# Performance work log

Hardware: AMD Instinct MI355X
Metric: run time of the kernel (lower is better)

The kernel has to match this reference:

```python
import jax, jax.numpy as jnp
import numpy as np

B, S, D = 2, 2048, 1024
E, K, F = 8, 2, 4 * 1024  # num_experts, top_k, fc_rate*embed_dim
T = B * S


def setup_inputs() -> dict:
    key = jax.random.key(0)
    ks = jax.random.split(key, 8)
    w = lambda k, shape: jax.random.normal(k, shape, jnp.float32) * 0.02
    return {
        "hidden_states": jax.random.normal(ks[0], (B, S, D), jnp.float32),
        "noise": jax.random.normal(ks[1], (T, E), jnp.float32),  # randn_like in router
        "Wg": w(ks[2], (D, E)), "bg": jnp.zeros((E,), jnp.float32),
        "Wn": w(ks[3], (D, E)), "bn": jnp.zeros((E,), jnp.float32),
        "W1": w(ks[4], (E, D, F)), "b1": jnp.zeros((E, F), jnp.float32),
        "W2": w(ks[5], (E, F, D)), "b2": jnp.zeros((E, D), jnp.float32),
    }


def reference(hidden_states, noise, Wg, bg, Wn, bn, W1, b1, W2, b2):
    b, s, d = hidden_states.shape
    x = hidden_states.reshape(-1, d)  # [T, D]

    # --- NoisyTopkRouter ---
    gate_logits = x @ Wg + bg                        # [T, E]
    noise_logits = x @ Wn + bn                       # [T, E]
    noisy_logits = gate_logits + noise * jax.nn.softplus(noise_logits)
    rw = jax.nn.softmax(noisy_logits.astype(jnp.float32), axis=-1)
    top_w, top_i = jax.lax.top_k(rw, K)              # [T, K]
    top_w = top_w / top_w.sum(-1, keepdims=True)
    top_w = top_w.astype(x.dtype)

    # Dense per-token combine coefficients: coef[t,e] = sum_k top_w[t,k]*[top_i[t,k]==e]
    tok = jnp.arange(x.shape[0])[:, None]
    coef = jnp.zeros((x.shape[0], E), x.dtype).at[tok, top_i].add(top_w)  # [T, E]

    # --- Experts: Linear -> GELU(exact) -> Linear (dropout = identity, eval mode) ---
    h = jax.nn.gelu(jnp.einsum('td,edf->tef', x, W1) + b1, approximate=False)  # [T,E,F]
    y = jnp.einsum('tef,efd->ted', h, W2) + b2                                  # [T,E,D]
    out = jnp.einsum('ted,te->td', y, coef)                                     # [T,D]

    return out.reshape(b, s, d), noisy_logits, gate_logits
```

## Files before the change

kernel.cpp:

```cpp
#include <hip/hip_runtime.h>
#include <hip/hip_bf16.h>

#define T_TOK 4096
#define D_DIM 1024
#define E_NUM 8
#define F_DIM 4096
#define NPAIR 8192

#define BM 128
#define BN 128
#define BK 64

typedef float f32x4 __attribute__((ext_vector_type(4)));
typedef __bf16 bf16x8 __attribute__((ext_vector_type(8)));
typedef unsigned short u16x8 __attribute__((ext_vector_type(8)));

__device__ __forceinline__ unsigned short f2bf(float f) {
    unsigned int u = __float_as_uint(f);
    u += 0x7fffu + ((u >> 16) & 1u);
    return (unsigned short)(u >> 16);
}

typedef const __attribute__((address_space(1))) void GV;
typedef __attribute__((address_space(3))) void LV;

__device__ __forceinline__ void load_lds16(const void* g, void* l) {
    __builtin_amdgcn_global_load_lds((GV*)g, (LV*)l, 16, 0, 0);
}

__device__ __forceinline__ bf16x8 lds_frag(const unsigned short* S, int row, int cs) {
    int byte = row * (BK * 2) + ((cs * 2) ^ ((row & 7) << 4));
    return *(const bf16x8*)((const char*)S + byte);
}

__global__ __launch_bounds__(256) void router_kernel(
    const float* __restrict__ x, const float* __restrict__ noise,
    const float* __restrict__ Wg, const float* __restrict__ bg,
    const float* __restrict__ Wn, const float* __restrict__ bn,
    float* __restrict__ out_noisy, float* __restrict__ out_gate,
    int* __restrict__ tk_idx, float* __restrict__ tk_w)
{
    int lane = threadIdx.x & 63;
    int t = blockIdx.x * 4 + (threadIdx.x >> 6);
    const float* xr = x + (size_t)t * D_DIM;

    float ag[E_NUM] = {}, an[E_NUM] = {};
    for (int it = 0; it < D_DIM / 64; ++it) {
        int d = it * 64 + lane;
        float xv = xr[d];
        float4 g0 = *(const float4*)(Wg + (size_t)d * E_NUM);
        float4 g1 = *(const float4*)(Wg + (size_t)d * E_NUM + 4);
        float4 m0 = *(const float4*)(Wn + (size_t)d * E_NUM);
        float4 m1 = *(const float4*)(Wn + (size_t)d * E_NUM + 4);
        ag[0] += xv * g0.x; ag[1] += xv * g0.y; ag[2] += xv * g0.z; ag[3] += xv * g0.w;
        ag[4] += xv * g1.x; ag[5] += xv * g1.y; ag[6] += xv * g1.z; ag[7] += xv * g1.w;
        an[0] += xv * m0.x; an[1] += xv * m0.y; an[2] += xv * m0.z; an[3] += xv * m0.w;
        an[4] += xv * m1.x; an[5] += xv * m1.y; an[6] += xv * m1.z; an[7] += xv * m1.w;
    }
    #pragma unroll
    for (int off = 32; off > 0; off >>= 1) {
        #pragma unroll
        for (int e = 0; e < E_NUM; ++e) {
            ag[e] += __shfl_xor(ag[e], off);
            an[e] += __shfl_xor(an[e], off);
        }
    }
    if (lane == 0) {
        float nz[E_NUM];
        #pragma unroll
        for (int e = 0; e < E_NUM; ++e) {
            float g = ag[e] + bg[e];
            float nn = an[e] + bn[e];
            float sp = fmaxf(nn, 0.f) + log1pf(expf(-fabsf(nn)));
            float z = g + noise[(size_t)t * E_NUM + e] * sp;
            out_gate[(size_t)t * E_NUM + e] = g;
            out_noisy[(size_t)t * E_NUM + e] = z;
            nz[e] = z;
        }
        int e0 = 0;
        #pragma unroll
        for (int e = 1; e < E_NUM; ++e) if (nz[e] > nz[e0]) e0 = e;
        int e1 = (e0 == 0) ? 1 : 0;
        #pragma unroll
        for (int e = 0; e < E_NUM; ++e) if (e != e0 && nz[e] > nz[e1]) e1 = e;
        float b = expf(nz[e1] - nz[e0]);
        float w0 = 1.f / (1.f + b);
        float w1 = b / (1.f + b);
        tk_idx[t * 2] = e0;  tk_idx[t * 2 + 1] = e1;
        tk_w[t * 2] = w0;    tk_w[t * 2 + 1] = w1;
    }
}

__global__ __launch_bounds__(256) void scan_scatter_kernel(
    const int* __restrict__ tk_idx,
    int* __restrict__ perm, int* __restrict__ meta)
{
    __shared__ int cnt[256][E_NUM];
    __shared__ int soff[E_NUM];
    int tid = threadIdx.x;
    const int PPT = NPAIR / 256;
    int p0 = tid * PPT;

    int c[E_NUM] = {};
    for (int i = 0; i < PPT; ++i) c[tk_idx[p0 + i]]++;
    #pragma unroll
    for (int e = 0; e < E_NUM; ++e) cnt[tid][e] = c[e];
    __syncthreads();

    if (tid < E_NUM) {
        int s = 0;
        for (int j = 0; j < 256; ++j) { int v = cnt[j][tid]; cnt[j][tid] = s; s += v; }
        soff[tid] = s;
    }
    __syncthreads();

    if (tid == 0) {
        int off = 0, nt = 0;
        for (int e = 0; e < E_NUM; ++e) {
            int ce = soff[e];
            meta[1 + e] = off;
            meta[9 + e] = ce;
            for (int j = 0; j < ce; j += BM) {
                meta[32 + nt]  = e;
                meta[160 + nt] = off + j;
                meta[288 + nt] = off + ce;
                nt++;
            }
            off += ce;
        }
        meta[0] = nt;
    }
    __syncthreads();
    if (tid < E_NUM) soff[tid] = meta[1 + tid];
    __syncthreads();

    int pos[E_NUM];
    #pragma unroll
    for (int e = 0; e < E_NUM; ++e) pos[e] = soff[e] + cnt[tid][e];
    for (int i = 0; i < PPT; ++i) {
        int e = tk_idx[p0 + i];
        perm[pos[e]++] = p0 + i;
    }
}

__global__ __launch_bounds__(256) void convert_x_kernel(
    const float* __restrict__ x, unsigned short* __restrict__ xb)
{
    size_t i = ((size_t)blockIdx.x * 256 + threadIdx.x) * 8;
    float4 a = *(const float4*)(x + i);
    float4 b = *(const float4*)(x + i + 4);
    u16x8 o;
    o[0] = f2bf(a.x); o[1] = f2bf(a.y); o[2] = f2bf(a.z); o[3] = f2bf(a.w);
    o[4] = f2bf(b.x); o[5] = f2bf(b.y); o[6] = f2bf(b.z); o[7] = f2bf(b.w);
    *(u16x8*)(xb + i) = o;
}

__global__ __launch_bounds__(256) void transpose_kernel(
    const float* __restrict__ W, unsigned short* __restrict__ WT, int R, int C)
{
    __shared__ float tile[32][33];
    int e = blockIdx.z;
    int c0 = blockIdx.x * 32, r0 = blockIdx.y * 32;
    int tx = threadIdx.x & 31, ty = threadIdx.x >> 5;
    const float* src = W + (size_t)e * R * C;
    #pragma unroll
    for (int i = 0; i < 4; ++i)
        tile[ty + 8 * i][tx] = src[(size_t)(r0 + ty + 8 * i) * C + c0 + tx];
    __syncthreads();
    unsigned short* dst = WT + (size_t)e * C * R;
    #pragma unroll
    for (int i = 0; i < 4; ++i)
        dst[(size_t)(c0 + ty + 8 * i) * R + r0 + tx] = f2bf(tile[tx][ty + 8 * i]);
}

__global__ __launch_bounds__(256, 4) void fc1_kernel(
    const unsigned short* __restrict__ xb,
    const unsigned short* __restrict__ W1T,
    const float* __restrict__ b1,
    const int* __restrict__ perm,
    const int* __restrict__ meta,
    unsigned short* __restrict__ h)
{
    const int nwg = 71 * (F_DIM / BN);
    const int cpx = nwg >> 3;
    int bid = blockIdx.x;
    int wg = (bid & 7) * cpx + (bid >> 3);
    int tile = wg >> 5;
    int n0 = (wg & 31) * BN;
    if (tile >= meta[0]) return;
    int e    = meta[32 + tile];
    int rs   = meta[160 + tile];
    int rend = meta[288 + tile];

    __shared__ __align__(16) unsigned short As[BM * BK];
    __shared__ __align__(16) unsigned short Bs[BN * BK];

    int tid = threadIdx.x, lane = tid & 63, wv = tid >> 6;
    int wm = (wv >> 1) * 64, wn = (wv & 1) * 64;
    int csw = ((tid & 7) ^ ((tid >> 3) & 7)) * 8;

    const unsigned short* asrc[4];
    #pragma unroll
    for (int i = 0; i < 4; ++i) {
        int q = tid + i * 256;
        int pos = rs + (q >> 3); if (pos >= NPAIR) pos = NPAIR - 1;
        int t = perm[pos] >> 1;
        asrc[i] = xb + (size_t)t * D_DIM + csw;
    }
    const unsigned short* bbase = W1T + ((size_t)e * F_DIM + n0 + wv * 32 + (lane >> 3)) * D_DIM + csw;

    f32x4 acc[4][4] = {};

    const int NT = D_DIM / BK;
    for (int t = 0; t < NT; ++t) {
        int k0 = t * BK;
        #pragma unroll
        for (int i = 0; i < 4; ++i)
            load_lds16(asrc[i] + k0, &As[(wv * 64 + i * 256) * 8]);
        #pragma unroll
        for (int j = 0; j < 4; ++j)
            load_lds16(bbase + (size_t)(j * 8) * D_DIM + k0, &Bs[(wv * 32 + j * 8) * BK]);
        asm volatile("s_waitcnt vmcnt(0)" ::: "memory");
        __builtin_amdgcn_s_barrier();
        #pragma unroll
        for (int kk = 0; kk < BK; kk += 32) {
            bf16x8 af[4], bf[4];
            #pragma unroll
            for (int m = 0; m < 4; ++m)
                af[m] = lds_frag(As, wm + m * 16 + (lane & 15), kk + (lane >> 4) * 8);
            #pragma unroll
            for (int n = 0; n < 4; ++n)
                bf[n] = lds_frag(Bs, wn + n * 16 + (lane & 15), kk + (lane >> 4) * 8);
            #pragma unroll
            for (int m = 0; m < 4; ++m)
                #pragma unroll
                for (int n = 0; n < 4; ++n)
                    acc[m][n] = __builtin_amdgcn_mfma_f32_16x16x32_bf16(af[m], bf[n], acc[m][n], 0, 0, 0);
        }
        asm volatile("s_waitcnt lgkmcnt(0)" ::: "memory");
        __builtin_amdgcn_s_barrier();
    }

    #pragma unroll
    for (int m = 0; m < 4; ++m) {
        #pragma unroll
        for (int j = 0; j < 4; ++j) {
            int r = wm + m * 16 + (lane >> 4) * 4 + j;
            int pos = rs + r;
            if (pos >= rend) continue;
            #pragma unroll
            for (int n = 0; n < 4; ++n) {
                int col = n0 + wn + n * 16 + (lane & 15);
                float v = acc[m][n][j] + b1[e * F_DIM + col];
                v = 0.5f * v * (1.f + erff(v * 0.70710678118654752f));
                h[(size_t)pos * F_DIM + col] = f2bf(v);
            }
        }
    }
}

__global__ __launch_bounds__(256, 4) void fc2_kernel(
    const unsigned short* __restrict__ h,
    const unsigned short* __restrict__ W2T,
    const float* __restrict__ b2,
    const int* __restrict__ perm,
    const float* __restrict__ tk_w,
    const int* __restrict__ meta,
    float* __restrict__ out)
{
    const int nwg = 71 * (D_DIM / BN) * 2;
    const int cpx = nwg >> 3;
    int bid = blockIdx.x;
    int wg = (bid & 7) * cpx + (bid >> 3);
    int tile = wg >> 4;
    int rem  = wg & 15;
    int n0 = (rem >> 1) * BN;
    int ks = rem & 1;
    if (tile >= meta[0]) return;
    int e    = meta[32 + tile];
    int rs   = meta[160 + tile];
    int rend = meta[288 + tile];
    int kbeg = ks * (F_DIM / 2);

    __shared__ __align__(16) unsigned short As[BM * BK];
    __shared__ __align__(16) unsigned short Bs[BN * BK];

    int tid = threadIdx.x, lane = tid & 63, wv = tid >> 6;
    int wm = (wv >> 1) * 64, wn = (wv & 1) * 64;
    int csw = ((tid & 7) ^ ((tid >> 3) & 7)) * 8;

    const unsigned short* asrc[4];
    #pragma unroll
    for (int i = 0; i < 4; ++i) {
        int q = tid + i * 256;
        int pos = rs + (q >> 3); if (pos >= NPAIR) pos = NPAIR - 1;
        asrc[i] = h + (size_t)pos * F_DIM + kbeg + csw;
    }
    const unsigned short* bbase = W2T + ((size_t)e * D_DIM + n0 + wv * 32 + (lane >> 3)) * F_DIM
                                + kbeg + csw;

    f32x4 acc[4][4] = {};

    const int NT = (F_DIM / 2) / BK;
    for (int t = 0; t < NT; ++t) {
        int k0 = t * BK;
        #pragma unroll
        for (int i = 0; i < 4; ++i)
            load_lds16(asrc[i] + k0, &As[(wv * 64 + i * 256) * 8]);
        #pragma unroll
        for (int j = 0; j < 4; ++j)
            load_lds16(bbase + (size_t)(j * 8) * F_DIM + k0, &Bs[(wv * 32 + j * 8) * BK]);
        asm volatile("s_waitcnt vmcnt(0)" ::: "memory");
        __builtin_amdgcn_s_barrier();
        #pragma unroll
        for (int kk = 0; kk < BK; kk += 32) {
            bf16x8 af[4], bf[4];
            #pragma unroll
            for (int m = 0; m < 4; ++m)
                af[m] = lds_frag(As, wm + m * 16 + (lane & 15), kk + (lane >> 4) * 8);
            #pragma unroll
            for (int n = 0; n < 4; ++n)
                bf[n] = lds_frag(Bs, wn + n * 16 + (lane & 15), kk + (lane >> 4) * 8);
            #pragma unroll
            for (int m = 0; m < 4; ++m)
                #pragma unroll
                for (int n = 0; n < 4; ++n)
                    acc[m][n] = __builtin_amdgcn_mfma_f32_16x16x32_bf16(af[m], bf[n], acc[m][n], 0, 0, 0);
        }
        asm volatile("s_waitcnt lgkmcnt(0)" ::: "memory");
        __builtin_amdgcn_s_barrier();
    }

    #pragma unroll
    for (int m = 0; m < 4; ++m) {
        #pragma unroll
        for (int j = 0; j < 4; ++j) {
            int r = wm + m * 16 + (lane >> 4) * 4 + j;
            int pos = rs + r;
            if (pos >= rend) continue;
            int pr = perm[pos];
            int t = pr >> 1;
            float w = tk_w[pr];
            #pragma unroll
            for (int n = 0; n < 4; ++n) {
                int col = n0 + wn + n * 16 + (lane & 15);
                float base = (ks == 0) ? b2[e * D_DIM + col] : 0.f;
                float v = (acc[m][n][j] + base) * w;
                atomicAdd(&out[(size_t)t * D_DIM + col], v);
            }
        }
    }
}

extern "C" void kernel_launch(void* const* d_in, const int* in_sizes, int n_in,
                              void* d_out, int out_size, void* d_ws, size_t ws_size,
                              hipStream_t stream)
{
    const float* x     = (const float*)d_in[0];
    const float* noise = (const float*)d_in[1];
    const float* Wg    = (const float*)d_in[2];
    const float* bg    = (const float*)d_in[3];
    const float* Wn    = (const float*)d_in[4];
    const float* bn    = (const float*)d_in[5];
    const float* W1    = (const float*)d_in[6];
    const float* b1    = (const float*)d_in[7];
    const float* W2    = (const float*)d_in[8];
    const float* b2    = (const float*)d_in[9];

    float* out       = (float*)d_out;
    float* out_noisy = out + (size_t)T_TOK * D_DIM;
    float* out_gate  = out_noisy + (size_t)T_TOK * E_NUM;

    char* ws = (char*)d_ws;
    int*   tk_idx = (int*)ws;
    float* tk_w   = (float*)(ws + 32768);
    int*   perm   = (int*)(ws + 65536);
    int*   meta   = (int*)(ws + 98304);
    size_t off = 131072;
    unsigned short* xb   = (unsigned short*)(ws + off); off += (size_t)T_TOK * D_DIM * 2;
    unsigned short* W1T  = (unsigned short*)(ws + off); off += (size_t)E_NUM * F_DIM * D_DIM * 2;
    unsigned short* W2T  = (unsigned short*)(ws + off); off += (size_t)E_NUM * D_DIM * F_DIM * 2;
    unsigned short* hbuf = (unsigned short*)(ws + off); off += (size_t)NPAIR * F_DIM * 2;

    hipMemsetAsync(d_out, 0, (size_t)out_size * sizeof(float), stream);

    router_kernel<<<T_TOK / 4, 256, 0, stream>>>(x, noise, Wg, bg, Wn, bn,
                                                 out_noisy, out_gate, tk_idx, tk_w);
    scan_scatter_kernel<<<1, 256, 0, stream>>>(tk_idx, perm, meta);
    convert_x_kernel<<<(T_TOK * D_DIM) / (256 * 8), 256, 0, stream>>>(x, xb);
    transpose_kernel<<<dim3(F_DIM / 32, D_DIM / 32, E_NUM), 256, 0, stream>>>(W1, W1T, D_DIM, F_DIM);
    transpose_kernel<<<dim3(D_DIM / 32, F_DIM / 32, E_NUM), 256, 0, stream>>>(W2, W2T, F_DIM, D_DIM);

    fc1_kernel<<<71 * (F_DIM / BN), 256, 0, stream>>>(xb, W1T, b1, perm, meta, hbuf);
    fc2_kernel<<<71 * (D_DIM / BN) * 2, 256, 0, stream>>>(hbuf, W2T, b2, perm, tk_w, meta, out);
}
```

Measured before the change: 478.3 us.

## Enlarge expert GEMM tiles to 256x256 with 512-thread blocks and reorder tile mapping

The fc1 and fc2 grouped GEMMs move from 128x128 tiles with 256 threads to 256x256 tiles with 512 threads (8 waves, each wave computing 128x64). The goal is to raise arithmetic intensity and cut redundant global and LDS traffic for the weights and gathered activations. Workgroup-to-tile mapping now iterates tiles fastest within each column chunk, and the grid is sized from a fixed maximum tile count (NTMAX). The trade-offs are fewer blocks per CU, higher register pressure from the 8x4 accumulators, and more wasted rows in partially filled expert tiles. The transpose launches are also reordered.

```diff
diff --git a/kernel.cpp b/kernel.cpp
--- a/kernel.cpp
+++ b/kernel.cpp
@@ -7,9 +7,10 @@
 #define F_DIM 4096
 #define NPAIR 8192
 
-#define BM 128
-#define BN 128
+#define BM 256
+#define BN 256
 #define BK 64
+#define NTMAX 39
 
 typedef float f32x4 __attribute__((ext_vector_type(4)));
 typedef __bf16 bf16x8 __attribute__((ext_vector_type(8)));
@@ -173,7 +174,7 @@
         dst[(size_t)(c0 + ty + 8 * i) * R + r0 + tx] = f2bf(tile[tx][ty + 8 * i]);
 }
 
-__global__ __launch_bounds__(256, 4) void fc1_kernel(
+__global__ __launch_bounds__(512, 2) void fc1_kernel(
     const unsigned short* __restrict__ xb,
     const unsigned short* __restrict__ W1T,
     const float* __restrict__ b1,
@@ -181,13 +182,13 @@
     const int* __restrict__ meta,
     unsigned short* __restrict__ h)
 {
-    const int nwg = 71 * (F_DIM / BN);
-    const int cpx = nwg >> 3;
+    int nt = meta[0];
     int bid = blockIdx.x;
-    int wg = (bid & 7) * cpx + (bid >> 3);
-    int tile = wg >> 5;
-    int n0 = (wg & 31) * BN;
-    if (tile >= meta[0]) return;
+    int wg = (bid & 7) * (NTMAX * 16 / 8) + (bid >> 3);
+    if (wg >= nt * 16) return;
+    int n0i = wg / nt;
+    int tile = wg - n0i * nt;
+    int n0 = n0i * BN;
     int e    = meta[32 + tile];
     int rs   = meta[160 + tile];
     int rend = meta[288 + tile];
@@ -196,43 +197,45 @@
     __shared__ __align__(16) unsigned short Bs[BN * BK];
 
     int tid = threadIdx.x, lane = tid & 63, wv = tid >> 6;
-    int wm = (wv >> 1) * 64, wn = (wv & 1) * 64;
+    int wm = (wv >> 2) * 128, wn = (wv & 3) * 64;
     int csw = ((tid & 7) ^ ((tid >> 3) & 7)) * 8;
 
     const unsigned short* asrc[4];
+    const unsigned short* bsrc[4];
     #pragma unroll
     for (int i = 0; i < 4; ++i) {
-        int q = tid + i * 256;
-        int pos = rs + (q >> 3); if (pos >= NPAIR) pos = NPAIR - 1;
+        int q = tid + i * 512;
+        int row = q >> 3;
+        int pos = rs + row; if (pos >= NPAIR) pos = NPAIR - 1;
         int t = perm[pos] >> 1;
         asrc[i] = xb + (size_t)t * D_DIM + csw;
-    }
-    const unsigned short* bbase = W1T + ((size_t)e * F_DIM + n0 + wv * 32 + (lane >> 3)) * D_DIM + csw;
-
-    f32x4 acc[4][4] = {};
+        bsrc[i] = W1T + ((size_t)e * F_DIM + n0 + row) * D_DIM + csw;
+    }
+
+    f32x4 acc[8][4] = {};
 
     const int NT = D_DIM / BK;
     for (int t = 0; t < NT; ++t) {
         int k0 = t * BK;
         #pragma unroll
         for (int i = 0; i < 4; ++i)
-            load_lds16(asrc[i] + k0, &As[(wv * 64 + i * 256) * 8]);
-        #pragma unroll
-        for (int j = 0; j < 4; ++j)
-            load_lds16(bbase + (size_t)(j * 8) * D_DIM + k0, &Bs[(wv * 32 + j * 8) * BK]);
+            load_lds16(asrc[i] + k0, &As[(tid + i * 512) * 8]);
+        #pragma unroll
+        for (int i = 0; i < 4; ++i)
+            load_lds16(bsrc[i] + k0, &Bs[(tid + i * 512) * 8]);
         asm volatile("s_waitcnt vmcnt(0)" ::: "memory");
         __builtin_amdgcn_s_barrier();
         #pragma unroll
         for (int kk = 0; kk < BK; kk += 32) {
-            bf16x8 af[4], bf[4];
-            #pragma unroll
-            for (int m = 0; m < 4; ++m)
+            bf16x8 af[8], bf[4];
+            #pragma unroll
+            for (int m = 0; m < 8; ++m)
                 af[m] = lds_frag(As, wm + m * 16 + (lane & 15), kk + (lane >> 4) * 8);
             #pragma unroll
             for (int n = 0; n < 4; ++n)
                 bf[n] = lds_frag(Bs, wn + n * 16 + (lane & 15), kk + (lane >> 4) * 8);
             #pragma unroll
-            for (int m = 0; m < 4; ++m)
+            for (int m = 0; m < 8; ++m)
                 #pragma unroll
                 for (int n = 0; n < 4; ++n)
                     acc[m][n] = __builtin_amdgcn_mfma_f32_16x16x32_bf16(af[m], bf[n], acc[m][n], 0, 0, 0);
@@ -242,7 +245,7 @@
     }
 
     #pragma unroll
-    for (int m = 0; m < 4; ++m) {
+    for (int m = 0; m < 8; ++m) {
         #pragma unroll
         for (int j = 0; j < 4; ++j) {
             int r = wm + m * 16 + (lane >> 4) * 4 + j;
@@ -259,7 +262,7 @@
     }
 }
 
-__global__ __launch_bounds__(256, 4) void fc2_kernel(
+__global__ __launch_bounds__(512, 2) void fc2_kernel(
     const unsigned short* __restrict__ h,
     const unsigned short* __restrict__ W2T,
     const float* __restrict__ b2,
@@ -268,61 +271,61 @@
     const int* __restrict__ meta,
     float* __restrict__ out)
 {
-    const int nwg = 71 * (D_DIM / BN) * 2;
-    const int cpx = nwg >> 3;
+    int nt = meta[0];
     int bid = blockIdx.x;
-    int wg = (bid & 7) * cpx + (bid >> 3);
-    int tile = wg >> 4;
-    int rem  = wg & 15;
-    int n0 = (rem >> 1) * BN;
-    int ks = rem & 1;
-    if (tile >= meta[0]) return;
+    int wg = (bid & 7) * (NTMAX * 8 / 8) + (bid >> 3);
+    if (wg >= nt * 8) return;
+    int cidx = wg / nt;
+    int tile = wg - cidx * nt;
+    int n0 = (cidx >> 1) * BN;
+    int ks = cidx & 1;
+    int kbeg = ks * (F_DIM / 2);
     int e    = meta[32 + tile];
     int rs   = meta[160 + tile];
     int rend = meta[288 + tile];
-    int kbeg = ks * (F_DIM / 2);
 
     __shared__ __align__(16) unsigned short As[BM * BK];
     __shared__ __align__(16) unsigned short Bs[BN * BK];
 
     int tid = threadIdx.x, lane = tid & 63, wv = tid >> 6;
-    int wm = (wv >> 1) * 64, wn = (wv & 1) * 64;
+    int wm = (wv >> 2) * 128, wn = (wv & 3) * 64;
     int csw = ((tid & 7) ^ ((tid >> 3) & 7)) * 8;
 
     const unsigned short* asrc[4];
+    const unsigned short* bsrc[4];
     #pragma unroll
     for (int i = 0; i < 4; ++i) {
-        int q = tid + i * 256;
-        int pos = rs + (q >> 3); if (pos >= NPAIR) pos = NPAIR - 1;
+        int q = tid + i * 512;
+        int row = q >> 3;
+        int pos = rs + row; if (pos >= NPAIR) pos = NPAIR - 1;
         asrc[i] = h + (size_t)pos * F_DIM + kbeg + csw;
-    }
-    const unsigned short* bbase = W2T + ((size_t)e * D_DIM + n0 + wv * 32 + (lane >> 3)) * F_DIM
-                                + kbeg + csw;
-
-    f32x4 acc[4][4] = {};
+        bsrc[i] = W2T + ((size_t)e * D_DIM + n0 + row) * F_DIM + kbeg + csw;
+    }
+
+    f32x4 acc[8][4] = {};
 
     const int NT = (F_DIM / 2) / BK;
     for (int t = 0; t < NT; ++t) {
         int k0 = t * BK;
         #pragma unroll
         for (int i = 0; i < 4; ++i)
-            load_lds16(asrc[i] + k0, &As[(wv * 64 + i * 256) * 8]);
-        #pragma unroll
-        for (int j = 0; j < 4; ++j)
-            load_lds16(bbase + (size_t)(j * 8) * F_DIM + k0, &Bs[(wv * 32 + j * 8) * BK]);
+            load_lds16(asrc[i] + k0, &As[(tid + i * 512) * 8]);
+        #pragma unroll
+        for (int i = 0; i < 4; ++i)
+            load_lds16(bsrc[i] + k0, &Bs[(tid + i * 512) * 8]);
         asm volatile("s_waitcnt vmcnt(0)" ::: "memory");
         __builtin_amdgcn_s_barrier();
         #pragma unroll
         for (int kk = 0; kk < BK; kk += 32) {
-            bf16x8 af[4], bf[4];
-            #pragma unroll
-            for (int m = 0; m < 4; ++m)
+            bf16x8 af[8], bf[4];
+            #pragma unroll
+            for (int m = 0; m < 8; ++m)
                 af[m] = lds_frag(As, wm + m * 16 + (lane & 15), kk + (lane >> 4) * 8);
             #pragma unroll
             for (int n = 0; n < 4; ++n)
                 bf[n] = lds_frag(Bs, wn + n * 16 + (lane & 15), kk + (lane >> 4) * 8);
             #pragma unroll
-            for (int m = 0; m < 4; ++m)
+            for (int m = 0; m < 8; ++m)
                 #pragma unroll
                 for (int n = 0; n < 4; ++n)
                     acc[m][n] = __builtin_amdgcn_mfma_f32_16x16x32_bf16(af[m], bf[n], acc[m][n], 0, 0, 0);
@@ -332,7 +335,7 @@
     }
 
     #pragma unroll
-    for (int m = 0; m < 4; ++m) {
+    for (int m = 0; m < 8; ++m) {
         #pragma unroll
         for (int j = 0; j < 4; ++j) {
             int r = wm + m * 16 + (lane >> 4) * 4 + j;
@@ -388,9 +391,9 @@
                                                  out_noisy, out_gate, tk_idx, tk_w);
     scan_scatter_kernel<<<1, 256, 0, stream>>>(tk_idx, perm, meta);
     convert_x_kernel<<<(T_TOK * D_DIM) / (256 * 8), 256, 0, stream>>>(x, xb);
+    transpose_kernel<<<dim3(D_DIM / 32, F_DIM / 32, E_NUM), 256, 0, stream>>>(W2, W2T, F_DIM, D_DIM);
     transpose_kernel<<<dim3(F_DIM / 32, D_DIM / 32, E_NUM), 256, 0, stream>>>(W1, W1T, D_DIM, F_DIM);
-    transpose_kernel<<<dim3(D_DIM / 32, F_DIM / 32, E_NUM), 256, 0, stream>>>(W2, W2T, F_DIM, D_DIM);
-
-    fc1_kernel<<<71 * (F_DIM / BN), 256, 0, stream>>>(xb, W1T, b1, perm, meta, hbuf);
-    fc2_kernel<<<71 * (D_DIM / BN) * 2, 256, 0, stream>>>(hbuf, W2T, b2, perm, tk_w, meta, out);
-}
+
+    fc1_kernel<<<NTMAX * 16, 512, 0, stream>>>(xb, W1T, b1, perm, meta, hbuf);
+    fc2_kernel<<<NTMAX * 8, 512, 0, stream>>>(hbuf, W2T, b2, perm, tk_w, meta, out);
+}
```

Result: slower. 663.5 us (+38.7%).
